# Kernel optimization log

Hardware: AMD Instinct MI355X
Metric: run time of the kernel (lower is better)

## Reference

```python
import jax, jax.numpy as jnp
import numpy as np

PAD_LABEL = 15
NUM_TAGS = 15


def setup_inputs() -> dict:
    key = jax.random.key(0)
    k1, k2, k3 = jax.random.split(key, 3)
    B, T, C = 4096, 512, NUM_TAGS
    logits = jax.random.normal(k1, (B, T, C), dtype=jnp.float32)
    y_true = jax.random.randint(k2, (B, T), 0, PAD_LABEL + 1, dtype=jnp.int32)
    # CRF transition matrix (learned param), glorot-ish scale
    transitions = jax.random.normal(k3, (C, C), dtype=jnp.float32) * 0.25
    return {"logits": logits, "y_true": y_true, "transitions": transitions}


def _log_norm(logits, transitions, mask):
    # logits: (B, T, C) float32, mask: (B, T) bool
    alpha0 = logits[:, 0, :]                       # (B, C)
    # scan over timesteps 1..T-1
    emits = jnp.swapaxes(logits[:, 1:, :], 0, 1)    # (T-1, B, C)
    masks = jnp.swapaxes(mask[:, 1:], 0, 1)         # (T-1, B)

    def step(alpha, inp):
        emit_t, mask_t = inp                        # (B, C), (B,)
        # scores[b, i, j] = alpha[b, i] + trans[i, j] + emit_t[b, j]
        scores = alpha[:, :, None] + transitions[None, :, :] + emit_t[:, None, :]
        new_alpha = jax.scipy.special.logsumexp(scores, axis=1)  # (B, C)
        alpha = jnp.where(mask_t[:, None], new_alpha, alpha)
        return alpha, None

    alpha, _ = jax.lax.scan(step, alpha0, (emits, masks))
    return jax.scipy.special.logsumexp(alpha, axis=1)  # (B,)


def _sequence_score(logits, transitions, labels, mask):
    mask_f = mask.astype(jnp.float32)
    safe_labels = jnp.where(mask, labels, 0)                    # (B, T)
    # emission scores along gold path
    em = jnp.take_along_axis(logits, safe_labels[:, :, None], axis=2)[:, :, 0]
    emission_score = jnp.sum(em * mask_f, axis=1)               # (B,)
    # transition scores between consecutive valid positions
    prev, curr = safe_labels[:, :-1], safe_labels[:, 1:]
    tmask_f = (mask[:, 1:] & mask[:, :-1]).astype(jnp.float32)
    trans_scores = transitions[prev, curr]                      # (B, T-1)
    transition_score = jnp.sum(trans_scores * tmask_f, axis=1)  # (B,)
    return emission_score + transition_score


def reference(logits, y_true, transitions):
    mask = y_true != PAD_LABEL                                  # (B, T) bool
    logZ = _log_norm(logits, transitions, mask)
    path_score = _sequence_score(logits, transitions, y_true, mask)
    nll = jnp.clip(logZ - path_score, 0.0, 1000000.0)
    return jnp.mean(nll)
```

## Files before the change

### kernel.cpp

```cpp
#include <hip/hip_runtime.h>

#define L2E  1.4426950408889634f
#define LN2f 0.6931471805599453f

template<int CTRL>
__device__ __forceinline__ float dppf(float x) {
  int r = __builtin_amdgcn_update_dpp(0, __builtin_bit_cast(int, x), CTRL, 0xF, 0xF, true);
  return __builtin_bit_cast(float, r);
}
template<int CTRL>
__device__ __forceinline__ int dppi(int x) {
  return __builtin_amdgcn_update_dpp(0, x, CTRL, 0xF, 0xF, true);
}

__device__ __forceinline__ float bflymax16(float x) {
  x = fmaxf(x, dppf<0xB1>(x));
  x = fmaxf(x, dppf<0x4E>(x));
  x = fmaxf(x, dppf<0x141>(x));
  x = fmaxf(x, dppf<0x140>(x));
  return x;
}

#define DOT(shv, tot) {                                   \
    float t0_ = (shv) * Wror[0], t1_ = 0.f, t2_ = 0.f, t3_ = 0.f; \
    t1_ = fmaf(dppf<0x121>(shv), Wror[1],  t1_);          \
    t2_ = fmaf(dppf<0x122>(shv), Wror[2],  t2_);          \
    t3_ = fmaf(dppf<0x123>(shv), Wror[3],  t3_);          \
    t0_ = fmaf(dppf<0x124>(shv), Wror[4],  t0_);          \
    t1_ = fmaf(dppf<0x125>(shv), Wror[5],  t1_);          \
    t2_ = fmaf(dppf<0x126>(shv), Wror[6],  t2_);          \
    t3_ = fmaf(dppf<0x127>(shv), Wror[7],  t3_);          \
    t0_ = fmaf(dppf<0x128>(shv), Wror[8],  t0_);          \
    t1_ = fmaf(dppf<0x129>(shv), Wror[9],  t1_);          \
    t2_ = fmaf(dppf<0x12A>(shv), Wror[10], t2_);          \
    t3_ = fmaf(dppf<0x12B>(shv), Wror[11], t3_);          \
    t0_ = fmaf(dppf<0x12C>(shv), Wror[12], t0_);          \
    t1_ = fmaf(dppf<0x12D>(shv), Wror[13], t1_);          \
    t2_ = fmaf(dppf<0x12E>(shv), Wror[14], t2_);          \
    t3_ = fmaf(dppf<0x12F>(shv), Wror[15], t3_);          \
    tot = (t0_ + t1_) + (t2_ + t3_); }

template<bool BWD>
__device__ __forceinline__ void scan(const float* __restrict__ ep,
                                     const int* __restrict__ ys,
                                     const float (&Wror)[16],
                                     int j, int jm,
                                     float& ownO, float& MO, float& eaccO) {
  float own, M, eacc;
  float ebuf[8]; int ybuf[8];
  const float* pe;
  const int* py;
  if (!BWD) {
    const float a0 = ep[0];
    const int y0 = ys[0];
    eacc = (y0 == jm) ? a0 : 0.f;
    const float A = (j < 15) ? a0 * L2E : -1.0e30f;
    const float M0 = bflymax16(A);
    own = exp2f(A - M0);
    M = M0;
    #pragma unroll
    for (int i = 0; i < 8; ++i) { ebuf[i] = ep[(1 + i) * 15]; ybuf[i] = ys[1 + i]; }
    pe = ep + 9 * 15;
    py = ys + 9;
  } else {
    eacc = 0.f;
    own = (j < 15) ? 1.f : 0.f;
    M = 0.f;
    #pragma unroll
    for (int i = 0; i < 8; ++i) { ebuf[i] = ep[(511 - i) * 15]; ybuf[i] = ys[511 - i]; }
    pe = ep + (511 - 8) * 15;
    py = ys + (511 - 8);
  }

  if (!BWD) {
    for (int sb = 0; sb < 31; ++sb) {
      #pragma unroll
      for (int k = 0; k < 8; ++k) {
        const float emit = ebuf[k]; const int yv = ybuf[k];
        ebuf[k] = *pe; pe += 15;
        ybuf[k] = *py; py += 1;
        const float p = exp2f(emit * L2E);
        float tot; DOT(own, tot);
        const float cand = tot * p;
        own = (yv != 15) ? cand : own;
        eacc += (yv == jm) ? emit : 0.f;
        if (k == 7) {
          const float m = bflymax16(own);
          own *= __builtin_amdgcn_rcpf(m);
          M += log2f(m);
        }
      }
    }
    #pragma unroll
    for (int k = 0; k < 7; ++k) {
      const float emit = ebuf[k]; const int yv = ybuf[k];
      ebuf[k] = *pe; pe += 15;
      const float p = exp2f(emit * L2E);
      float tot; DOT(own, tot);
      const float cand = tot * p;
      own = (yv != 15) ? cand : own;
      eacc += (yv == jm) ? emit : 0.f;
    }
  } else {
    for (int sb = 0; sb < 32; ++sb) {
      #pragma unroll
      for (int k = 0; k < 8; ++k) {
        const float emit = ebuf[k]; const int yv = ybuf[k];
        ebuf[k] = *pe; pe -= 15;
        ybuf[k] = *py; py -= 1;
        const float p = exp2f(emit * L2E);
        const float share = own * p;
        float tot; DOT(share, tot);
        own = (yv != 15) ? tot : own;
        eacc += (yv == jm) ? emit : 0.f;
        if (k == 7) {
          const float m = bflymax16(own);
          own *= __builtin_amdgcn_rcpf(m);
          M += log2f(m);
        }
      }
    }
  }
  ownO = own; MO = M; eaccO = eacc;
}

__global__ __launch_bounds__(256, 2)
void crf_rot(const float* __restrict__ logits, const int* __restrict__ yg,
             const float* __restrict__ trans, float* __restrict__ out) {
  __shared__ float Tl[240];
  __shared__ int   yl[8 * 520];
  __shared__ float comb[8][2][16];
  __shared__ float pathE[8][2];
  __shared__ float transS[8];
  __shared__ float blks[8];

  const int tid = threadIdx.x;
  if (tid < 225) Tl[tid] = trans[tid];
  {
    const int4* src = (const int4*)(yg + (size_t)blockIdx.x * 4096);
    int4* dst = (int4*)yl;
    #pragma unroll
    for (int k = 0; k < 4; ++k) {
      const int g = tid + k * 256;
      const int sq = g >> 7, pos = g & 127;
      dst[sq * 130 + pos] = src[g];
    }
  }
  __syncthreads();

  {
    const int q = tid >> 5, l32 = tid & 31;
    const int* ys = yl + q * 520;
    float acc = 0.f;
    #pragma unroll
    for (int m = 0; m < 16; ++m) {
      const int t = 1 + l32 + 32 * m;
      if (t < 512) {
        const int yc = ys[t], yp = ys[t - 1];
        if (yc < 15 && yp < 15) acc += Tl[yp * 15 + yc];
      }
    }
    #pragma unroll
    for (int k = 1; k < 32; k <<= 1) acc += __shfl_xor(acc, k, 32);
    if (l32 == 0) transS[q] = acc;
  }

  const int wave = tid >> 6, lane = tid & 63;
  const int j = lane & 15;
  const int sLoc = (wave >> 1) * 4 + (lane >> 4);
  const bool isFwd = (wave & 1) == 0;
  const int seq = blockIdx.x * 8 + sLoc;
  const int jj = (j < 15) ? j : 14;
  const int jm = (j < 15) ? j : 255;
  const float* ep = logits + (size_t)seq * 7680 + jj;
  const int* ys = yl + sLoc * 520;

  float Wror[16];
  Wror[0] = (j < 15) ? exp2f(Tl[j * 16] * L2E) : 0.f;
#define SETW(R) { const int s_ = dppi<0x120 + (R)>(j);                  \
    const bool v_ = (j < 15) && (s_ < 15);                              \
    const int ix_ = isFwd ? s_ * 15 + j : j * 15 + s_;                  \
    Wror[R] = v_ ? exp2f(Tl[ix_] * L2E) : 0.f; }
  SETW(1)  SETW(2)  SETW(3)  SETW(4)  SETW(5)
  SETW(6)  SETW(7)  SETW(8)  SETW(9)  SETW(10)
  SETW(11) SETW(12) SETW(13) SETW(14) SETW(15)
#undef SETW
  #pragma unroll
  for (int r = 0; r < 16; ++r) asm volatile("" : "+v"(Wror[r]));

  float own, M, eacc;
  if (isFwd) scan<false>(ep, ys, Wror, j, jm, own, M, eacc);
  else       scan<true >(ep, ys, Wror, j, jm, own, M, eacc);

  const int dir = isFwd ? 0 : 1;
  if (j < 15) comb[sLoc][dir][j] = M + log2f(own);
  #pragma unroll
  for (int k = 1; k < 16; k <<= 1) eacc += __shfl_xor(eacc, k, 16);
  if (j == 0) pathE[sLoc][dir] = eacc;

  __syncthreads();

  if (tid < 8) {
    float mx = -3.0e38f; float s[15];
    #pragma unroll
    for (int i = 0; i < 15; ++i) {
      s[i] = comb[tid][0][i] + comb[tid][1][i];
      mx = fmaxf(mx, s[i]);
    }
    float sum = 0.f;
    #pragma unroll
    for (int i = 0; i < 15; ++i) sum += exp2f(s[i] - mx);
    const float logZ = (mx + log2f(sum)) * LN2f;
    const float path = pathE[tid][0] + pathE[tid][1] + transS[tid];
    float nll = logZ - path;
    nll = fminf(fmaxf(nll, 0.f), 1000000.f);
    blks[tid] = nll;
  }
  __syncthreads();
  if (tid == 0) {
    float tot = (blks[0] + blks[1]) + (blks[2] + blks[3]) +
                (blks[4] + blks[5]) + (blks[6] + blks[7]);
    atomicAdd(out, tot * (1.0f / 4096.0f));
  }
}

extern "C" void kernel_launch(void* const* d_in, const int* in_sizes, int n_in,
                              void* d_out, int out_size, void* d_ws, size_t ws_size,
                              hipStream_t stream) {
  const float* logits = (const float*)d_in[0];
  const int*   y      = (const int*)d_in[1];
  const float* trans  = (const float*)d_in[2];
  float* out = (float*)d_out;

  hipMemsetAsync(out, 0, sizeof(float), stream);

  const int B = in_sizes[1] / 512;
  crf_rot<<<dim3(B / 8), dim3(256), 0, stream>>>(logits, y, trans, out);
}
```

Baseline: 63.55 us.

## Split each sequence's 16-wide transition dot across 32 lanes with swizzle combine

Each sequence direction now uses 32 lanes instead of 16. Each half-row of 16 lanes computes 8 of the 16 transition products, and the two partial sums are combined with a ds_swizzle across the halves. This roughly halves the serial dependency chain and the weight registers per step, and doubles the blocks with higher launch-bounds occupancy. In exchange it adds a swizzle per step, duplicates the emission loads and exp work across the halves, and halves the sequences per block.

```diff
diff --git a/kernel.cpp b/kernel.cpp
--- a/kernel.cpp
+++ b/kernel.cpp
@@ -11,6 +11,11 @@
 template<int CTRL>
 __device__ __forceinline__ int dppi(int x) {
   return __builtin_amdgcn_update_dpp(0, x, CTRL, 0xF, 0xF, true);
+}
+
+__device__ __forceinline__ float swz16(float x) {
+  return __builtin_bit_cast(float,
+      __builtin_amdgcn_ds_swizzle(__builtin_bit_cast(int, x), 0x401F));
 }
 
 __device__ __forceinline__ float bflymax16(float x) {
@@ -22,28 +27,22 @@
 }
 
 #define DOT(shv, tot) {                                   \
-    float t0_ = (shv) * Wror[0], t1_ = 0.f, t2_ = 0.f, t3_ = 0.f; \
-    t1_ = fmaf(dppf<0x121>(shv), Wror[1],  t1_);          \
-    t2_ = fmaf(dppf<0x122>(shv), Wror[2],  t2_);          \
-    t3_ = fmaf(dppf<0x123>(shv), Wror[3],  t3_);          \
-    t0_ = fmaf(dppf<0x124>(shv), Wror[4],  t0_);          \
-    t1_ = fmaf(dppf<0x125>(shv), Wror[5],  t1_);          \
-    t2_ = fmaf(dppf<0x126>(shv), Wror[6],  t2_);          \
-    t3_ = fmaf(dppf<0x127>(shv), Wror[7],  t3_);          \
-    t0_ = fmaf(dppf<0x128>(shv), Wror[8],  t0_);          \
-    t1_ = fmaf(dppf<0x129>(shv), Wror[9],  t1_);          \
-    t2_ = fmaf(dppf<0x12A>(shv), Wror[10], t2_);          \
-    t3_ = fmaf(dppf<0x12B>(shv), Wror[11], t3_);          \
-    t0_ = fmaf(dppf<0x12C>(shv), Wror[12], t0_);          \
-    t1_ = fmaf(dppf<0x12D>(shv), Wror[13], t1_);          \
-    t2_ = fmaf(dppf<0x12E>(shv), Wror[14], t2_);          \
-    t3_ = fmaf(dppf<0x12F>(shv), Wror[15], t3_);          \
-    tot = (t0_ + t1_) + (t2_ + t3_); }
+    const float b_ = hsel ? dppf<0x128>(shv) : (shv);     \
+    float t0_ = b_ * Wr[0];                               \
+    float t1_ = dppf<0x121>(b_) * Wr[1];                  \
+    t0_ = fmaf(dppf<0x122>(b_), Wr[2], t0_);              \
+    t1_ = fmaf(dppf<0x123>(b_), Wr[3], t1_);              \
+    t0_ = fmaf(dppf<0x124>(b_), Wr[4], t0_);              \
+    t1_ = fmaf(dppf<0x125>(b_), Wr[5], t1_);              \
+    t0_ = fmaf(dppf<0x126>(b_), Wr[6], t0_);              \
+    t1_ = fmaf(dppf<0x127>(b_), Wr[7], t1_);              \
+    const float part_ = t0_ + t1_;                        \
+    tot = part_ + swz16(part_); }
 
 template<bool BWD>
 __device__ __forceinline__ void scan(const float* __restrict__ ep,
                                      const int* __restrict__ ys,
-                                     const float (&Wror)[16],
+                                     const float (&Wr)[8], bool hsel,
                                      int j, int jm,
                                      float& ownO, float& MO, float& eaccO) {
   float own, M, eacc;
@@ -124,23 +123,23 @@
   ownO = own; MO = M; eaccO = eacc;
 }
 
-__global__ __launch_bounds__(256, 2)
-void crf_rot(const float* __restrict__ logits, const int* __restrict__ yg,
-             const float* __restrict__ trans, float* __restrict__ out) {
+__global__ __launch_bounds__(256, 4)
+void crf_rot32(const float* __restrict__ logits, const int* __restrict__ yg,
+               const float* __restrict__ trans, float* __restrict__ out) {
   __shared__ float Tl[240];
-  __shared__ int   yl[8 * 520];
-  __shared__ float comb[8][2][16];
-  __shared__ float pathE[8][2];
-  __shared__ float transS[8];
-  __shared__ float blks[8];
+  __shared__ int   yl[4 * 520];
+  __shared__ float comb[4][2][16];
+  __shared__ float pathE[4][2];
+  __shared__ float transS[4];
+  __shared__ float blks[4];
 
   const int tid = threadIdx.x;
   if (tid < 225) Tl[tid] = trans[tid];
   {
-    const int4* src = (const int4*)(yg + (size_t)blockIdx.x * 4096);
+    const int4* src = (const int4*)(yg + (size_t)blockIdx.x * 2048);
     int4* dst = (int4*)yl;
     #pragma unroll
-    for (int k = 0; k < 4; ++k) {
+    for (int k = 0; k < 2; ++k) {
       const int g = tid + k * 256;
       const int sq = g >> 7, pos = g & 127;
       dst[sq * 130 + pos] = src[g];
@@ -149,58 +148,65 @@
   __syncthreads();
 
   {
-    const int q = tid >> 5, l32 = tid & 31;
+    const int q = tid >> 6, l64 = tid & 63;
     const int* ys = yl + q * 520;
     float acc = 0.f;
     #pragma unroll
-    for (int m = 0; m < 16; ++m) {
-      const int t = 1 + l32 + 32 * m;
+    for (int m = 0; m < 8; ++m) {
+      const int t = 1 + l64 + 64 * m;
       if (t < 512) {
         const int yc = ys[t], yp = ys[t - 1];
         if (yc < 15 && yp < 15) acc += Tl[yp * 15 + yc];
       }
     }
     #pragma unroll
-    for (int k = 1; k < 32; k <<= 1) acc += __shfl_xor(acc, k, 32);
-    if (l32 == 0) transS[q] = acc;
+    for (int k = 1; k < 64; k <<= 1) acc += __shfl_xor(acc, k, 64);
+    if (l64 == 0) transS[q] = acc;
   }
 
   const int wave = tid >> 6, lane = tid & 63;
+  const int c = lane >> 5;
+  const bool hsel = ((lane >> 4) & 1) != 0;
   const int j = lane & 15;
-  const int sLoc = (wave >> 1) * 4 + (lane >> 4);
+  const int sLoc = (wave >> 1) * 2 + c;
   const bool isFwd = (wave & 1) == 0;
-  const int seq = blockIdx.x * 8 + sLoc;
+  const int seq = blockIdx.x * 4 + sLoc;
   const int jj = (j < 15) ? j : 14;
   const int jm = (j < 15) ? j : 255;
   const float* ep = logits + (size_t)seq * 7680 + jj;
   const int* ys = yl + sLoc * 520;
 
-  float Wror[16];
-  Wror[0] = (j < 15) ? exp2f(Tl[j * 16] * L2E) : 0.f;
-#define SETW(R) { const int s_ = dppi<0x120 + (R)>(j);                  \
+  const int jr8 = dppi<0x128>(j);
+  const int hb = hsel ? jr8 : j;
+  float Wr[8];
+  {
+    const int s_ = hb;
+    const bool v_ = (j < 15) && (s_ < 15);
+    const int ix_ = isFwd ? s_ * 15 + j : j * 15 + s_;
+    Wr[0] = v_ ? exp2f(Tl[v_ ? ix_ : 0] * L2E) : 0.f;
+  }
+#define SETW(K) { const int s_ = dppi<0x120 + (K)>(hb);                 \
     const bool v_ = (j < 15) && (s_ < 15);                              \
     const int ix_ = isFwd ? s_ * 15 + j : j * 15 + s_;                  \
-    Wror[R] = v_ ? exp2f(Tl[ix_] * L2E) : 0.f; }
-  SETW(1)  SETW(2)  SETW(3)  SETW(4)  SETW(5)
-  SETW(6)  SETW(7)  SETW(8)  SETW(9)  SETW(10)
-  SETW(11) SETW(12) SETW(13) SETW(14) SETW(15)
+    Wr[K] = v_ ? exp2f(Tl[v_ ? ix_ : 0] * L2E) : 0.f; }
+  SETW(1) SETW(2) SETW(3) SETW(4) SETW(5) SETW(6) SETW(7)
 #undef SETW
   #pragma unroll
-  for (int r = 0; r < 16; ++r) asm volatile("" : "+v"(Wror[r]));
+  for (int r = 0; r < 8; ++r) asm volatile("" : "+v"(Wr[r]));
 
   float own, M, eacc;
-  if (isFwd) scan<false>(ep, ys, Wror, j, jm, own, M, eacc);
-  else       scan<true >(ep, ys, Wror, j, jm, own, M, eacc);
+  if (isFwd) scan<false>(ep, ys, Wr, hsel, j, jm, own, M, eacc);
+  else       scan<true >(ep, ys, Wr, hsel, j, jm, own, M, eacc);
 
   const int dir = isFwd ? 0 : 1;
-  if (j < 15) comb[sLoc][dir][j] = M + log2f(own);
+  if (!hsel && j < 15) comb[sLoc][dir][j] = M + log2f(own);
   #pragma unroll
   for (int k = 1; k < 16; k <<= 1) eacc += __shfl_xor(eacc, k, 16);
-  if (j == 0) pathE[sLoc][dir] = eacc;
+  if (!hsel && j == 0) pathE[sLoc][dir] = eacc;
 
   __syncthreads();
 
-  if (tid < 8) {
+  if (tid < 4) {
     float mx = -3.0e38f; float s[15];
     #pragma unroll
     for (int i = 0; i < 15; ++i) {
@@ -218,8 +224,7 @@
   }
   __syncthreads();
   if (tid == 0) {
-    float tot = (blks[0] + blks[1]) + (blks[2] + blks[3]) +
-                (blks[4] + blks[5]) + (blks[6] + blks[7]);
+    const float tot = (blks[0] + blks[1]) + (blks[2] + blks[3]);
     atomicAdd(out, tot * (1.0f / 4096.0f));
   }
 }
@@ -235,5 +240,5 @@
   hipMemsetAsync(out, 0, sizeof(float), stream);
 
   const int B = in_sizes[1] / 512;
-  crf_rot<<<dim3(B / 8), dim3(256), 0, stream>>>(logits, y, trans, out);
-}
+  crf_rot32<<<dim3(B / 4), dim3(256), 0, stream>>>(logits, y, trans, out);
+}
```

Result: slower. 79.89 us (+25.7%).
